# Performance work log

Hardware: AMD Instinct MI355X
Metric: run time of the kernel (lower is better)

Reference implementation:

```python
import jax, jax.numpy as jnp
import numpy as np
import math

B, S, D, H, L, K = 4, 2048, 256, 8, 2, 3  # batch, seq, dim, heads, MTA layers, conv kernel
HS = D // H
EPS = 1e-6


def layer_norm(x, g, b):
    m = jnp.mean(x, axis=-1, keepdims=True)
    v = jnp.mean((x - m) ** 2, axis=-1, keepdims=True)
    return (x - m) * jax.lax.rsqrt(v + EPS) * g + b


def temporal_encoder(x, W, b):
    # x: [B,S,D]; W: [L,K,D,D] (WIO), b: [L,D]. Stack of kernel-3 'SAME' Conv1d, GELU between.
    for i in range(L):
        x = jax.lax.conv_general_dilated(
            x, W[i], window_strides=(1,), padding=[(1, 1)],
            dimension_numbers=("NWC", "WIO", "NWC")) + b[i]
        if i < L - 1:
            x = jax.nn.gelu(x)
    return x


def setup_inputs() -> dict:
    key = jax.random.key(0)
    ks = jax.random.split(key, 10)
    w = lambda k, shape: jax.random.normal(k, shape, jnp.float32) * 0.02
    return {
        "x": jax.random.normal(ks[0], (B, S, D), jnp.float32),
        "ln1_g": jnp.ones((D,), jnp.float32), "ln1_b": jnp.zeros((D,), jnp.float32),
        "Wq": w(ks[1], (L, K, D, D)), "bq": jnp.zeros((L, D), jnp.float32),
        "Wk": w(ks[2], (L, K, D, D)), "bk": jnp.zeros((L, D), jnp.float32),
        "Wv": w(ks[3], (L, K, D, D)), "bv": jnp.zeros((L, D), jnp.float32),
        "ln2_g": jnp.ones((D,), jnp.float32), "ln2_b": jnp.zeros((D,), jnp.float32),
        "Wo1": w(ks[4], (D, D)), "bo1": jnp.zeros((D,), jnp.float32),
        "Wo2": w(ks[5], (D, D)), "bo2": jnp.zeros((D,), jnp.float32),
        "mask": jax.random.randint(ks[6], (B, S), 0, 2).astype(jnp.int32),
    }


def reference(x, ln1_g, ln1_b, Wq, bq, Wk, bk, Wv, bv, ln2_g, ln2_b, Wo1, bo1, Wo2, bo2, mask):
    b_, s_ = x.shape[0], x.shape[1]
    h = layer_norm(x, ln1_g, ln1_b)
    q = temporal_encoder(h, Wq, bq).reshape(b_, s_, H, HS)
    k = temporal_encoder(h, Wk, bk).reshape(b_, s_, H, HS)
    v = temporal_encoder(h, Wv, bv).reshape(b_, s_, H, HS)
    # attention scores [B,H,S,S]
    scores = jnp.einsum("bqhd,bkhd->bhqk", q, k) / math.sqrt(HS)
    m = mask[:, None, None, :].astype(scores.dtype)  # [B,1,1,S]
    scores = scores + (1.0 - m) * (-1e30)
    probs = jax.nn.softmax(scores, axis=-1)
    attn = jnp.einsum("bhqk,bkhd->bqhd", probs, v).reshape(b_, s_, D)
    residual = x + attn  # dropout p=0
    o = layer_norm(residual, ln2_g, ln2_b)
    o = jax.nn.gelu(o @ Wo1 + bo1)  # 1x1 Conv1D == per-token linear
    o = o @ Wo2 + bo2 + residual
    return o
```

## Files before the change

kernel.cpp:

```cpp
#include <hip/hip_runtime.h>
#include <hip/hip_bf16.h>
#include <math.h>

#define BB 4
#define SS 2048
#define DD 256
#define HH 8
#define HSZ 32

typedef __attribute__((ext_vector_type(8))) short short8;
typedef __attribute__((ext_vector_type(4))) float f32x4;

__device__ __forceinline__ void gload_lds16(const void* g, void* l) {
    __builtin_amdgcn_global_load_lds((const unsigned int*)g, (unsigned int*)l,
                                     16, 0, 0);
}

__device__ __forceinline__ float exp2_hw(float x) {
    float r;
    asm("v_exp_f32 %0, %1" : "=v"(r) : "v"(x));
    return r;
}

__device__ __forceinline__ unsigned int perm_pack(float a, float b, unsigned int sel) {
    unsigned int r;
    asm("v_perm_b32 %0, %1, %2, %3"
        : "=v"(r)
        : "v"(__float_as_uint(b)), "v"(__float_as_uint(a)), "s"(sel));
    return r;
}

__device__ __forceinline__ float gelu_f(float x) {
    float x3 = x * x * x;
    float z = 0.7978845608028654f * fmaf(0.044715f, x3, x);
    float e = __expf(2.0f * z);
    float t = 1.0f - 2.0f / (e + 1.0f);
    return 0.5f * x * (1.0f + t);
}

__device__ __forceinline__ unsigned short f2bf(float f) {
    unsigned int u = __float_as_uint(f);
    u = (u + 0x7fffu + ((u >> 16) & 1u)) >> 16;
    return (unsigned short)u;
}

template<bool HASRES>
__device__ __forceinline__ void ln_wave_body(
    int t, int lane,
    const float* __restrict__ x, const float* __restrict__ addin,
    const float* __restrict__ g, const float* __restrict__ bvec,
    float* __restrict__ resid_out, unsigned short* __restrict__ oln_bf)
{
    const int base = t * DD + lane * 4;
    float4 v4 = *(const float4*)&x[base];
    if (HASRES) {
        float4 a4 = *(const float4*)&addin[base];
        v4.x += a4.x; v4.y += a4.y; v4.z += a4.z; v4.w += a4.w;
        *(float4*)&resid_out[base] = v4;
    }
    float s = (v4.x + v4.y) + (v4.z + v4.w);
    #pragma unroll
    for (int o = 1; o < 64; o <<= 1) s += __shfl_xor(s, o);
    float mean = s * (1.0f / 256.0f);
    float dx = v4.x - mean, dy = v4.y - mean, dz = v4.z - mean, dw = v4.w - mean;
    float q = (dx * dx + dy * dy) + (dz * dz + dw * dw);
    #pragma unroll
    for (int o = 1; o < 64; o <<= 1) q += __shfl_xor(q, o);
    float r = rsqrtf(q * (1.0f / 256.0f) + 1e-6f);
    const float4 g4 = *(const float4*)&g[lane * 4];
    const float4 b4 = *(const float4*)&bvec[lane * 4];
    ushort4 o4;
    o4.x = f2bf(dx * r * g4.x + b4.x);
    o4.y = f2bf(dy * r * g4.y + b4.y);
    o4.z = f2bf(dz * r * g4.z + b4.z);
    o4.w = f2bf(dw * r * g4.w + b4.w);
    *(ushort4*)&oln_bf[base] = o4;
}

__global__ __launch_bounds__(256) void prep_kernel(
    const float* __restrict__ Wq, const float* __restrict__ Wk,
    const float* __restrict__ Wv, const float* __restrict__ Wo1,
    const float* __restrict__ Wo2, unsigned short* __restrict__ wt,
    const float* __restrict__ x, const float* __restrict__ ln1g,
    const float* __restrict__ ln1b, unsigned short* __restrict__ h_bf,
    const int* __restrict__ mask, float* __restrict__ maskf)
{
    if (blockIdx.x < 1280) {
        const int WCp = 3 * DD * DD;
        const int WMp = DD * DD;
        const float* src; unsigned short* dst; int rel;
        int i = blockIdx.x;
        if (i < 1152) {
            int seg = i / 192; rel = i % 192;
            src = seg == 0 ? Wq : seg == 1 ? Wq + WCp : seg == 2 ? Wk :
                  seg == 3 ? Wk + WCp : seg == 4 ? Wv : Wv + WCp;
            dst = wt + (size_t)seg * WCp;
        } else {
            int j = i - 1152; int seg = j / 64; rel = j % 64;
            src = seg == 0 ? Wo1 : Wo2;
            dst = wt + (size_t)6 * WCp + (size_t)seg * WMp;
        }
        __shared__ unsigned short t[32][33];
        const int tx = threadIdx.x & 31, ty = threadIdx.x >> 5;
        const int r0 = (rel / 8) * 32, c0 = (rel % 8) * 32;
        #pragma unroll
        for (int j = 0; j < 32; j += 8)
            t[ty + j][tx] = f2bf(src[(r0 + ty + j) * 256 + c0 + tx]);
        __syncthreads();
        #pragma unroll
        for (int j = 0; j < 32; j += 8) {
            unsigned int och = (unsigned int)(c0 + ty + j);
            unsigned int k   = (unsigned int)(r0 + tx);
            unsigned int u   = och * 32u + (k & 31u);
            u ^= ((u >> 6) & 7u) << 3;
            dst[(size_t)(k >> 5) * 8192 + u] = t[tx][ty + j];
        }
    } else if (blockIdx.x < 3328) {
        const int wv = threadIdx.x >> 6, lane = threadIdx.x & 63;
        ln_wave_body<false>((blockIdx.x - 1280) * 4 + wv, lane,
                            x, nullptr, ln1g, ln1b, nullptr, h_bf);
    } else {
        const float M_ON  = -8.0f * 1.4426950408889634f;
        const float M_OFF = -1.442695e30f;
        int i = (blockIdx.x - 3328) * 1024 + threadIdx.x * 4;
        int4 m4 = *(const int4*)&mask[i];
        float4 f4;
        f4.x = m4.x ? M_ON : M_OFF;
        f4.y = m4.y ? M_ON : M_OFF;
        f4.z = m4.z ? M_ON : M_OFF;
        f4.w = m4.w ? M_ON : M_OFF;
        *(float4*)&maskf[i] = f4;
    }
}

__global__ __launch_bounds__(256, 3) void convdual_kernel(
    const unsigned short* __restrict__ in,
    const unsigned short* __restrict__ W0a, const unsigned short* __restrict__ W0b,
    const unsigned short* __restrict__ W0c,
    const unsigned short* __restrict__ W1a, const unsigned short* __restrict__ W1b,
    const unsigned short* __restrict__ W1c,
    const float* __restrict__ ba, const float* __restrict__ bb,
    const float* __restrict__ bc,
    unsigned short* __restrict__ oQ, unsigned short* __restrict__ oK,
    unsigned short* __restrict__ oV, int S)
{
    constexpr int LDW = 264;
    __shared__ __align__(16) unsigned short stage[36 * LDW];
    __shared__ __align__(16) unsigned short wbuf[2][8192];

    unsigned short* const inter = stage;

    const int set = blockIdx.x % 3;
    const int tile = blockIdx.x / 3;
    const unsigned short* W0 = set == 0 ? W0a : (set == 1 ? W0b : W0c);
    const unsigned short* W1 = set == 0 ? W1a : (set == 1 ? W1b : W1c);
    const float* bias         = set == 0 ? ba  : (set == 1 ? bb  : bc);
    unsigned short* outp      = set == 0 ? oQ  : (set == 1 ? oK  : oV);

    const int tid = threadIdx.x;
    const int lane = tid & 63, wv = tid >> 6;
    const int lm = lane & 15, lq = lane >> 4;
    const int tpb = S / 32;
    const int b = tile / tpb;
    const int s0 = (tile % tpb) * 32;
    const int NC = S / 32;
    const int c = s0 >> 5;

    for (int i = tid; i < 36 * 32; i += 256) {
        int r = i >> 5, c8 = (i & 31) << 3;
        int s = s0 + r - 2;
        int4 val = make_int4(0, 0, 0, 0);
        if (s >= 0 && s < S)
            val = *(const int4*)&in[(size_t)(b * S + s) * 256 + c8];
        *(int4*)&stage[r * LDW + c8] = val;
    }

    const int n0 = wv * 64;

    const int wq = wv * 4096;
    const char* w0p = (const char*)W0 + wq + lane * 16;
    const char* w1p = (const char*)W1 + wq + lane * 16;
    char* const wb0 = (char*)wbuf;

    unsigned int boff[4];
    #pragma unroll
    for (int nt = 0; nt < 4; ++nt) {
        unsigned int och = (unsigned int)(n0 + nt * 16 + lm);
        unsigned int R = och * 64u + (unsigned int)lq * 16u;
        boff[nt] = R ^ (((R >> 7) & 7u) << 4);
    }

    __syncthreads();

    {
        f32x4 acc[3][4];
        #pragma unroll
        for (int mt = 0; mt < 3; ++mt)
            #pragma unroll
            for (int nt = 0; nt < 4; ++nt) acc[mt][nt] = (f32x4){0.f, 0.f, 0.f, 0.f};

        #pragma unroll
        for (int j = 0; j < 4; ++j) gload_lds16(w0p + j * 1024,         wb0 + wq + j * 1024);
        #pragma unroll
        for (int j = 0; j < 4; ++j) gload_lds16(w0p + 16384 + j * 1024, wb0 + 16384 + wq + j * 1024);

        short8 a0c, a1c, a2c;
        {
            const int icc0 = lq * 8;
            int r20 = 32 + lm; r20 = r20 > 35 ? 35 : r20;
            a0c = *(const short8*)&stage[lm * LDW + icc0];
            a1c = *(const short8*)&stage[(16 + lm) * LDW + icc0];
            a2c = *(const short8*)&stage[r20 * LDW + icc0];
        }

        asm volatile("s_waitcnt vmcnt(4)" ::: "memory");
        __builtin_amdgcn_sched_barrier(0);
        short8 bfc[4];
        #pragma unroll
        for (int nt = 0; nt < 4; ++nt)
            bfc[nt] = *(const short8*)(wb0 + boff[nt]);

        #pragma unroll
        for (int it = 0; it < 24; ++it) {
            asm volatile("s_waitcnt lgkmcnt(0)" ::: "memory");
            __builtin_amdgcn_sched_barrier(0);
            if (it + 2 < 24) {
                char* ld = wb0 + ((it & 1) << 14) + wq;
                const int soff = (it + 2) * 16384;
                #pragma unroll
                for (int j = 0; j < 4; ++j)
                    gload_lds16(w0p + soff + j * 1024, ld + j * 1024);
            }
            __builtin_amdgcn_sched_barrier(0);

            __builtin_amdgcn_s_setprio(1);
            #pragma unroll
            for (int nt = 0; nt < 4; ++nt) {
                acc[0][nt] = __builtin_amdgcn_mfma_f32_16x16x32_bf16(a0c, bfc[nt], acc[0][nt], 0, 0, 0);
                acc[1][nt] = __builtin_amdgcn_mfma_f32_16x16x32_bf16(a1c, bfc[nt], acc[1][nt], 0, 0, 0);
                acc[2][nt] = __builtin_amdgcn_mfma_f32_16x16x32_bf16(a2c, bfc[nt], acc[2][nt], 0, 0, 0);
            }
            __builtin_amdgcn_s_setprio(0);
            __builtin_amdgcn_sched_barrier(0);

            if (it + 1 < 24) {
                if (it + 2 < 24) { asm volatile("s_waitcnt vmcnt(4)" ::: "memory"); }
                else             { asm volatile("s_waitcnt vmcnt(0)" ::: "memory"); }
                __builtin_amdgcn_sched_barrier(0);
                const char* wb = wb0 + (((it + 1) & 1) << 14);
                #pragma unroll
                for (int nt = 0; nt < 4; ++nt)
                    bfc[nt] = *(const short8*)(wb + boff[nt]);
                const int kk = (it + 1) >> 3;
                const int icc = ((it + 1) & 7) * 32 + lq * 8;
                int r2 = kk + 32 + lm; r2 = r2 > 35 ? 35 : r2;
                a0c = *(const short8*)&stage[(kk + lm) * LDW + icc];
                a1c = *(const short8*)&stage[(kk + 16 + lm) * LDW + icc];
                a2c = *(const short8*)&stage[r2 * LDW + icc];
            }
        }

        __syncthreads();

        #pragma unroll
        for (int j = 0; j < 4; ++j) gload_lds16(w1p + j * 1024,         wb0 + wq + j * 1024);
        #pragma unroll
        for (int j = 0; j < 4; ++j) gload_lds16(w1p + 16384 + j * 1024, wb0 + 16384 + wq + j * 1024);

        #pragma unroll
        for (int mt = 0; mt < 3; ++mt)
            #pragma unroll
            for (int nt = 0; nt < 4; ++nt) {
                int ch = n0 + nt * 16 + lm;
                float bv = bias[ch];
                #pragma unroll
                for (int r = 0; r < 4; ++r) {
                    int j = mt * 16 + lq * 4 + r;
                    if (j < 34) {
                        int token = s0 - 1 + j;
                        unsigned short v = (token >= 0 && token < S)
                            ? f2bf(gelu_f(acc[mt][nt][r] + bv)) : (unsigned short)0;
                        inter[j * LDW + ch] = v;
                    }
                }
            }
    }
    __syncthreads();

    f32x4 acc2[2][4];
    #pragma unroll
    for (int mt = 0; mt < 2; ++mt)
        #pragma unroll
        for (int nt = 0; nt < 4; ++nt) acc2[mt][nt] = (f32x4){0.f, 0.f, 0.f, 0.f};
    {
        char* const wb0 = (char*)wbuf;
        short8 a0c, a1c;
        {
            const int icc0 = lq * 8;
            a0c = *(const short8*)&inter[lm * LDW + icc0];
            a1c = *(const short8*)&inter[(16 + lm) * LDW + icc0];
        }

        asm volatile("s_waitcnt vmcnt(4)" ::: "memory");
        __builtin_amdgcn_sched_barrier(0);
        short8 bfc[4];
        #pragma unroll
        for (int nt = 0; nt < 4; ++nt)
            bfc[nt] = *(const short8*)(wb0 + boff[nt]);

        #pragma unroll
        for (int it = 0; it < 24; ++it) {
            asm volatile("s_waitcnt lgkmcnt(0)" ::: "memory");
            __builtin_amdgcn_sched_barrier(0);
            if (it + 2 < 24) {
                char* ld = wb0 + ((it & 1) << 14) + wq;
                const int soff = (it + 2) * 16384;
                #pragma unroll
                for (int j = 0; j < 4; ++j)
                    gload_lds16(w1p + soff + j * 1024, ld + j * 1024);
            }
            __builtin_amdgcn_sched_barrier(0);

            __builtin_amdgcn_s_setprio(1);
            #pragma unroll
            for (int nt = 0; nt < 4; ++nt) {
                acc2[0][nt] = __builtin_amdgcn_mfma_f32_16x16x32_bf16(a0c, bfc[nt], acc2[0][nt], 0, 0, 0);
                acc2[1][nt] = __builtin_amdgcn_mfma_f32_16x16x32_bf16(a1c, bfc[nt], acc2[1][nt], 0, 0, 0);
            }
            __builtin_amdgcn_s_setprio(0);
            __builtin_amdgcn_sched_barrier(0);

            if (it + 1 < 24) {
                if (it + 2 < 24) { asm volatile("s_waitcnt vmcnt(4)" ::: "memory"); }
                else             { asm volatile("s_waitcnt vmcnt(0)" ::: "memory"); }
                __builtin_amdgcn_sched_barrier(0);
                const char* wb = wb0 + (((it + 1) & 1) << 14);
                #pragma unroll
                for (int nt = 0; nt < 4; ++nt)
                    bfc[nt] = *(const short8*)(wb + boff[nt]);
                const int kk = (it + 1) >> 3;
                const int icc = ((it + 1) & 7) * 32 + lq * 8;
                a0c = *(const short8*)&inter[(kk + lm) * LDW + icc];
                a1c = *(const short8*)&inter[(kk + 16 + lm) * LDW + icc];
            }
        }
    }

    __syncthreads();
    if (set < 2) {
        #pragma unroll
        for (int mt = 0; mt < 2; ++mt)
            #pragma unroll
            for (int nt = 0; nt < 4; ++nt) {
                int o = n0 + nt * 16 + lm;
                int d = o & 31, h = o >> 5;
                float bv = bias[256 + o];
                #pragma unroll
                for (int r = 0; r < 4; ++r) {
                    int t = lq * 4 + r;
                    stage[mt * 4096 + (h * 64 + (d >> 3) * 16 + t) * 8 + (d & 7)] =
                        f2bf(acc2[mt][nt][r] + bv);
                }
            }
        __syncthreads();
        int h = tid >> 5;
        size_t base = ((size_t)(b * 8 + h) * NC + c) * 1024;
        #pragma unroll
        for (int half = 0; half < 2; ++half) {
            int4 v0 = *(const int4*)&stage[half * 4096 + tid * 16];
            int4 v1 = *(const int4*)&stage[half * 4096 + tid * 16 + 8];
            size_t dst = base + half * 512 + (tid & 31) * 16;
            *(int4*)&outp[dst] = v0;
            *(int4*)&outp[dst + 8] = v1;
        }
    } else {
        #pragma unroll
        for (int mt = 0; mt < 2; ++mt)
            #pragma unroll
            for (int nt = 0; nt < 4; ++nt) {
                int o = n0 + nt * 16 + lm;
                int d = o & 31, h = o >> 5;
                float bv = bias[256 + o];
                #pragma unroll
                for (int r = 0; r < 4; ++r) {
                    int t = lq * 4 + r;
                    stage[mt * 4096 +
                          ((h * 2 + (d >> 4)) * 32 + (t >> 3) * 16 + (d & 15)) * 8 + (t & 7)] =
                        f2bf(acc2[mt][nt][r] + bv);
                }
            }
        __syncthreads();
        int h = tid >> 5, dh = (tid >> 4) & 1;
        size_t base = ((size_t)(b * 8 + h) * NC + c) * 1024;
        #pragma unroll
        for (int half = 0; half < 2; ++half) {
            int4 v0 = *(const int4*)&stage[half * 4096 + tid * 16];
            int4 v1 = *(const int4*)&stage[half * 4096 + tid * 16 + 8];
            size_t dst = base + dh * 512 + half * 256 + (tid & 15) * 16;
            *(int4*)&outp[dst] = v0;
            *(int4*)&outp[dst + 8] = v1;
        }
    }
}

__global__ __launch_bounds__(256, 2) void tail_kernel(
    const float* __restrict__ x, const float* __restrict__ attn,
    const float* __restrict__ g2, const float* __restrict__ b2,
    const unsigned short* __restrict__ W1, const float* __restrict__ bo1,
    const unsigned short* __restrict__ W2, const float* __restrict__ bo2,
    float* __restrict__ out, int S)
{
    constexpr int LDW = 264;
    __shared__ __align__(16) unsigned short h_lds[16 * LDW];
    __shared__ __align__(16) unsigned short h2_lds[16 * LDW];
    __shared__ __align__(16) float resid_lds[16][DD];
    __shared__ __align__(16) unsigned short wbuf[2][8192];

    const int tid = threadIdx.x;
    const int lane = tid & 63, wv = tid >> 6;
    const int lm = lane & 15, lq = lane >> 4;
    const int t0 = blockIdx.x * 16;
    const int n0 = wv * 64;

    const int wq = wv * 4096;
    const char* w1p = (const char*)W1 + wq + lane * 16;
    const char* w2p = (const char*)W2 + wq + lane * 16;
    char* const wb0 = (char*)wbuf;

    unsigned int boff[4];
    #pragma unroll
    for (int nt = 0; nt < 4; ++nt) {
        unsigned int och = (unsigned int)(n0 + nt * 16 + lm);
        unsigned int R = och * 64u + (unsigned int)lq * 16u;
        boff[nt] = R ^ (((R >> 7) & 7u) << 4);
    }

    #pragma unroll
    for (int j = 0; j < 4; ++j) gload_lds16(w1p + j * 1024,         wb0 + wq + j * 1024);
    #pragma unroll
    for (int j = 0; j < 4; ++j) gload_lds16(w1p + 16384 + j * 1024, wb0 + 16384 + wq + j * 1024);

    #pragma unroll
    for (int j = 0; j < 4; ++j) {
        int t = wv * 4 + j;
        int base = (t0 + t) * DD + lane * 4;
        float4 v4 = *(const float4*)&x[base];
        float4 a4 = *(const float4*)&attn[base];
        v4.x += a4.x; v4.y += a4.y; v4.z += a4.z; v4.w += a4.w;
        *(float4*)&resid_lds[t][lane * 4] = v4;
        float s = (v4.x + v4.y) + (v4.z + v4.w);
        #pragma unroll
        for (int o = 1; o < 64; o <<= 1) s += __shfl_xor(s, o);
        float mean = s * (1.0f / 256.0f);
        float dx = v4.x - mean, dy = v4.y - mean, dz = v4.z - mean, dw = v4.w - mean;
        float q = (dx * dx + dy * dy) + (dz * dz + dw * dw);
        #pragma unroll
        for (int o = 1; o < 64; o <<= 1) q += __shfl_xor(q, o);
        float r = rsqrtf(q * (1.0f / 256.0f) + 1e-6f);
        const float4 g4 = *(const float4*)&g2[lane * 4];
        const float4 b4 = *(const float4*)&b2[lane * 4];
        ushort4 o4;
        o4.x = f2bf(dx * r * g4.x + b4.x);
        o4.y = f2bf(dy * r * g4.y + b4.y);
        o4.z = f2bf(dz * r * g4.z + b4.z);
        o4.w = f2bf(dw * r * g4.w + b4.w);
        *(ushort4*)&h_lds[t * LDW + lane * 4] = o4;
    }
    __syncthreads();

    {
        f32x4 acc[4];
        #pragma unroll
        for (int nt = 0; nt < 4; ++nt) acc[nt] = (f32x4){0.f, 0.f, 0.f, 0.f};

        short8 a0c = *(const short8*)&h_lds[lm * LDW + lq * 8];
        asm volatile("s_waitcnt vmcnt(4)" ::: "memory");
        __builtin_amdgcn_sched_barrier(0);
        short8 bfc[4];
        #pragma unroll
        for (int nt = 0; nt < 4; ++nt)
            bfc[nt] = *(const short8*)(wb0 + boff[nt]);

        #pragma unroll
        for (int it = 0; it < 8; ++it) {
            asm volatile("s_waitcnt lgkmcnt(0)" ::: "memory");
            __builtin_amdgcn_sched_barrier(0);
            if (it + 2 < 8) {
                char* ld = wb0 + ((it & 1) << 14) + wq;
                const int soff = (it + 2) * 16384;
                #pragma unroll
                for (int j = 0; j < 4; ++j)
                    gload_lds16(w1p + soff + j * 1024, ld + j * 1024);
            }
            __builtin_amdgcn_sched_barrier(0);

            __builtin_amdgcn_s_setprio(1);
            #pragma unroll
            for (int nt = 0; nt < 4; ++nt)
                acc[nt] = __builtin_amdgcn_mfma_f32_16x16x32_bf16(a0c, bfc[nt], acc[nt], 0, 0, 0);
            __builtin_amdgcn_s_setprio(0);
            __builtin_amdgcn_sched_barrier(0);

            if (it + 1 < 8) {
                if (it + 2 < 8) { asm volatile("s_waitcnt vmcnt(4)" ::: "memory"); }
                else            { asm volatile("s_waitcnt vmcnt(0)" ::: "memory"); }
                __builtin_amdgcn_sched_barrier(0);
                const char* wb = wb0 + (((it + 1) & 1) << 14);
                #pragma unroll
                for (int nt = 0; nt < 4; ++nt)
                    bfc[nt] = *(const short8*)(wb + boff[nt]);
                a0c = *(const short8*)&h_lds[lm * LDW + (it + 1) * 32 + lq * 8];
            }
        }

        asm volatile("s_waitcnt lgkmcnt(0)" ::: "memory");
        __builtin_amdgcn_sched_barrier(0);
        #pragma unroll
        for (int j = 0; j < 4; ++j) gload_lds16(w2p + j * 1024,         wb0 + wq + j * 1024);
        #pragma unroll
        for (int j = 0; j < 4; ++j) gload_lds16(w2p + 16384 + j * 1024, wb0 + 16384 + wq + j * 1024);

        #pragma unroll
        for (int nt = 0; nt < 4; ++nt) {
            int ch = n0 + nt * 16 + lm;
            float bv = bo1[ch];
            #pragma unroll
            for (int r = 0; r < 4; ++r) {
                int tok = lq * 4 + r;
                h2_lds[tok * LDW + ch] = f2bf(gelu_f(acc[nt][r] + bv));
            }
        }
    }
    __syncthreads();

    {
        f32x4 acc[4];
        #pragma unroll
        for (int nt = 0; nt < 4; ++nt) acc[nt] = (f32x4){0.f, 0.f, 0.f, 0.f};

        short8 a0c = *(const short8*)&h2_lds[lm * LDW + lq * 8];
        asm volatile("s_waitcnt vmcnt(4)" ::: "memory");
        __builtin_amdgcn_sched_barrier(0);
        short8 bfc[4];
        #pragma unroll
        for (int nt = 0; nt < 4; ++nt)
            bfc[nt] = *(const short8*)(wb0 + boff[nt]);

        #pragma unroll
        for (int it = 0; it < 8; ++it) {
            asm volatile("s_waitcnt lgkmcnt(0)" ::: "memory");
            __builtin_amdgcn_sched_barrier(0);
            if (it + 2 < 8) {
                char* ld = wb0 + ((it & 1) << 14) + wq;
                const int soff = (it + 2) * 16384;
                #pragma unroll
                for (int j = 0; j < 4; ++j)
                    gload_lds16(w2p + soff + j * 1024, ld + j * 1024);
            }
            __builtin_amdgcn_sched_barrier(0);

            __builtin_amdgcn_s_setprio(1);
            #pragma unroll
            for (int nt = 0; nt < 4; ++nt)
                acc[nt] = __builtin_amdgcn_mfma_f32_16x16x32_bf16(a0c, bfc[nt], acc[nt], 0, 0, 0);
            __builtin_amdgcn_s_setprio(0);
            __builtin_amdgcn_sched_barrier(0);

            if (it + 1 < 8) {
                if (it + 2 < 8) { asm volatile("s_waitcnt vmcnt(4)" ::: "memory"); }
                else            { asm volatile("s_waitcnt vmcnt(0)" ::: "memory"); }
                __builtin_amdgcn_sched_barrier(0);
                const char* wb = wb0 + (((it + 1) & 1) << 14);
                #pragma unroll
                for (int nt = 0; nt < 4; ++nt)
                    bfc[nt] = *(const short8*)(wb + boff[nt]);
                a0c = *(const short8*)&h2_lds[lm * LDW + (it + 1) * 32 + lq * 8];
            }
        }
        #pragma unroll
        for (int nt = 0; nt < 4; ++nt) {
            int ch = n0 + nt * 16 + lm;
            float bv = bo2[ch];
            #pragma unroll
            for (int r = 0; r < 4; ++r) {
                int tok = lq * 4 + r;
                out[(size_t)(t0 + tok) * DD + ch] = acc[nt][r] + bv + resid_lds[tok][ch];
            }
        }
    }
}

__global__ __launch_bounds__(256) void attn_mfma_kernel(
    const unsigned short* __restrict__ Qf, const unsigned short* __restrict__ Kf,
    const unsigned short* __restrict__ Vf, const float* __restrict__ maskf,
    float* __restrict__ Out, int S, int H)
{
    constexpr int LDP = 40;
    __shared__ __align__(16) unsigned short p_lds[4][2][16 * LDP];

    const int bh = ((blockIdx.x & 7) << 2) | ((blockIdx.x >> 3) & 3);
    const int qt = (blockIdx.x >> 5) * 128;
    const int b = bh / H;
    const int tid = threadIdx.x;
    const int lane = tid & 63, wv = tid >> 6;
    const int lm = lane & 15, lq = lane >> 4;
    const int q0 = qt + wv * 32;
    const int NC = S / 32;

    const size_t base = (size_t)bh * NC * 1024;
    const unsigned short* qp = &Qf[base + (size_t)(q0 >> 5) * 1024 + lane * 8];
    short8 qf0 = *(const short8*)(qp);
    short8 qf1 = *(const short8*)(qp + 512);
    const unsigned short* kp = Kf + base + lane * 8;
    const unsigned short* vp = Vf + base + lane * 8;

    short8 ones;
    #pragma unroll
    for (int j = 0; j < 8; ++j) ones[j] = (short)0x3F80;

    f32x4 o00 = {0.f, 0.f, 0.f, 0.f}, o01 = {0.f, 0.f, 0.f, 0.f};
    f32x4 o10 = {0.f, 0.f, 0.f, 0.f}, o11 = {0.f, 0.f, 0.f, 0.f};
    f32x4 lacc0 = {0.f, 0.f, 0.f, 0.f}, lacc1 = {0.f, 0.f, 0.f, 0.f};
    const f32x4 zf = {0.f, 0.f, 0.f, 0.f};

    const float scale2 = 0.17677669529663687f * 1.4426950408889634f;
    const unsigned int psel = 0x07060302u;
    const float* mp0 = maskf + b * S + lq * 4;
    const float* mp1 = mp0 + 16;

    unsigned short* pw0 = p_lds[wv][0];
    unsigned short* pw1 = p_lds[wv][1];
    const int pst = lm * LDP + lq * 4;
    const int prd = lm * LDP + lq * 8;

    short8 kA0 = *(const short8*)(kp);
    short8 kA1 = *(const short8*)(kp + 512);
    short8 vA0 = *(const short8*)(vp);
    short8 vA1 = *(const short8*)(vp + 512);
    short8 kB0, kB1, vB0, vB1;

    for (int c = 0; c < NC; c += 2) {
        {
            const unsigned short* kq = kp + (size_t)(c + 1) * 1024;
            const unsigned short* vq = vp + (size_t)(c + 1) * 1024;
            kB0 = *(const short8*)(kq);
            kB1 = *(const short8*)(kq + 512);
            vB0 = *(const short8*)(vq);
            vB1 = *(const short8*)(vq + 512);
        }

        {
            f32x4 s00 = __builtin_amdgcn_mfma_f32_16x16x32_bf16(kA0, qf0, zf, 0, 0, 0);
            f32x4 s01 = __builtin_amdgcn_mfma_f32_16x16x32_bf16(kA1, qf0, zf, 0, 0, 0);
            f32x4 s10 = __builtin_amdgcn_mfma_f32_16x16x32_bf16(kA0, qf1, zf, 0, 0, 0);
            f32x4 s11 = __builtin_amdgcn_mfma_f32_16x16x32_bf16(kA1, qf1, zf, 0, 0, 0);

            float4 mf0 = *(const float4*)(mp0 + c * 32);
            float4 mf1 = *(const float4*)(mp1 + c * 32);

            float p0[8], p1[8];
            p0[0] = exp2_hw(fmaf(s00[0], scale2, mf0.x));
            p0[1] = exp2_hw(fmaf(s00[1], scale2, mf0.y));
            p0[2] = exp2_hw(fmaf(s00[2], scale2, mf0.z));
            p0[3] = exp2_hw(fmaf(s00[3], scale2, mf0.w));
            p0[4] = exp2_hw(fmaf(s01[0], scale2, mf1.x));
            p0[5] = exp2_hw(fmaf(s01[1], scale2, mf1.y));
            p0[6] = exp2_hw(fmaf(s01[2], scale2, mf1.z));
            p0[7] = exp2_hw(fmaf(s01[3], scale2, mf1.w));
            p1[0] = exp2_hw(fmaf(s10[0], scale2, mf0.x));
            p1[1] = exp2_hw(fmaf(s10[1], scale2, mf0.y));
            p1[2] = exp2_hw(fmaf(s10[2], scale2, mf0.z));
            p1[3] = exp2_hw(fmaf(s10[3], scale2, mf0.w));
            p1[4] = exp2_hw(fmaf(s11[0], scale2, mf1.x));
            p1[5] = exp2_hw(fmaf(s11[1], scale2, mf1.y));
            p1[6] = exp2_hw(fmaf(s11[2], scale2, mf1.z));
            p1[7] = exp2_hw(fmaf(s11[3], scale2, mf1.w));

            uint2 w0, w1;
            w0.x = perm_pack(p0[0], p0[1], psel); w0.y = perm_pack(p0[2], p0[3], psel);
            w1.x = perm_pack(p0[4], p0[5], psel); w1.y = perm_pack(p0[6], p0[7], psel);
            *(uint2*)&pw0[pst] = w0;
            *(uint2*)&pw0[pst + 16] = w1;
            w0.x = perm_pack(p1[0], p1[1], psel); w0.y = perm_pack(p1[2], p1[3], psel);
            w1.x = perm_pack(p1[4], p1[5], psel); w1.y = perm_pack(p1[6], p1[7], psel);
            *(uint2*)&pw1[pst] = w0;
            *(uint2*)&pw1[pst + 16] = w1;

            short8 pA0 = *(const short8*)&pw0[prd];
            short8 pA1 = *(const short8*)&pw1[prd];

            lacc0 = __builtin_amdgcn_mfma_f32_16x16x32_bf16(pA0, ones, lacc0, 0, 0, 0);
            o00   = __builtin_amdgcn_mfma_f32_16x16x32_bf16(pA0, vA0, o00, 0, 0, 0);
            o01   = __builtin_amdgcn_mfma_f32_16x16x32_bf16(pA0, vA1, o01, 0, 0, 0);
            lacc1 = __builtin_amdgcn_mfma_f32_16x16x32_bf16(pA1, ones, lacc1, 0, 0, 0);
            o10   = __builtin_amdgcn_mfma_f32_16x16x32_bf16(pA1, vA0, o10, 0, 0, 0);
            o11   = __builtin_amdgcn_mfma_f32_16x16x32_bf16(pA1, vA1, o11, 0, 0, 0);
        }

        if (c + 2 < NC) {
            const unsigned short* kq = kp + (size_t)(c + 2) * 1024;
            const unsigned short* vq = vp + (size_t)(c + 2) * 1024;
            kA0 = *(const short8*)(kq);
            kA1 = *(const short8*)(kq + 512);
            vA0 = *(const short8*)(vq);
            vA1 = *(const short8*)(vq + 512);
        }

        {
            f32x4 s00 = __builtin_amdgcn_mfma_f32_16x16x32_bf16(kB0, qf0, zf, 0, 0, 0);
            f32x4 s01 = __builtin_amdgcn_mfma_f32_16x16x32_bf16(kB1, qf0, zf, 0, 0, 0);
            f32x4 s10 = __builtin_amdgcn_mfma_f32_16x16x32_bf16(kB0, qf1, zf, 0, 0, 0);
            f32x4 s11 = __builtin_amdgcn_mfma_f32_16x16x32_bf16(kB1, qf1, zf, 0, 0, 0);

            float4 mf0 = *(const float4*)(mp0 + (c + 1) * 32);
            float4 mf1 = *(const float4*)(mp1 + (c + 1) * 32);

            float p0[8], p1[8];
            p0[0] = exp2_hw(fmaf(s00[0], scale2, mf0.x));
            p0[1] = exp2_hw(fmaf(s00[1], scale2, mf0.y));
            p0[2] = exp2_hw(fmaf(s00[2], scale2, mf0.z));
            p0[3] = exp2_hw(fmaf(s00[3], scale2, mf0.w));
            p0[4] = exp2_hw(fmaf(s01[0], scale2, mf1.x));
            p0[5] = exp2_hw(fmaf(s01[1], scale2, mf1.y));
            p0[6] = exp2_hw(fmaf(s01[2], scale2, mf1.z));
            p0[7] = exp2_hw(fmaf(s01[3], scale2, mf1.w));
            p1[0] = exp2_hw(fmaf(s10[0], scale2, mf0.x));
            p1[1] = exp2_hw(fmaf(s10[1], scale2, mf0.y));
            p1[2] = exp2_hw(fmaf(s10[2], scale2, mf0.z));
            p1[3] = exp2_hw(fmaf(s10[3], scale2, mf0.w));
            p1[4] = exp2_hw(fmaf(s11[0], scale2, mf1.x));
            p1[5] = exp2_hw(fmaf(s11[1], scale2, mf1.y));
            p1[6] = exp2_hw(fmaf(s11[2], scale2, mf1.z));
            p1[7] = exp2_hw(fmaf(s11[3], scale2, mf1.w));

            uint2 w0, w1;
            w0.x = perm_pack(p0[0], p0[1], psel); w0.y = perm_pack(p0[2], p0[3], psel);
            w1.x = perm_pack(p0[4], p0[5], psel); w1.y = perm_pack(p0[6], p0[7], psel);
            *(uint2*)&pw0[pst] = w0;
            *(uint2*)&pw0[pst + 16] = w1;
            w0.x = perm_pack(p1[0], p1[1], psel); w0.y = perm_pack(p1[2], p1[3], psel);
            w1.x = perm_pack(p1[4], p1[5], psel); w1.y = perm_pack(p1[6], p1[7], psel);
            *(uint2*)&pw1[pst] = w0;
            *(uint2*)&pw1[pst + 16] = w1;

            short8 pA0 = *(const short8*)&pw0[prd];
            short8 pA1 = *(const short8*)&pw1[prd];

            lacc0 = __builtin_amdgcn_mfma_f32_16x16x32_bf16(pA0, ones, lacc0, 0, 0, 0);
            o00   = __builtin_amdgcn_mfma_f32_16x16x32_bf16(pA0, vB0, o00, 0, 0, 0);
            o01   = __builtin_amdgcn_mfma_f32_16x16x32_bf16(pA0, vB1, o01, 0, 0, 0);
            lacc1 = __builtin_amdgcn_mfma_f32_16x16x32_bf16(pA1, ones, lacc1, 0, 0, 0);
            o10   = __builtin_amdgcn_mfma_f32_16x16x32_bf16(pA1, vB0, o10, 0, 0, 0);
            o11   = __builtin_amdgcn_mfma_f32_16x16x32_bf16(pA1, vB1, o11, 0, 0, 0);
        }
    }

    #pragma unroll
    for (int r = 0; r < 4; ++r) {
        float inv0 = 1.0f / lacc0[r];
        size_t ob0 = (size_t)(b * S + q0 + lq * 4 + r) * 256 + (bh % H) * 32;
        Out[ob0 + lm] = o00[r] * inv0;
        Out[ob0 + 16 + lm] = o01[r] * inv0;
        float inv1 = 1.0f / lacc1[r];
        size_t ob1 = (size_t)(b * S + q0 + 16 + lq * 4 + r) * 256 + (bh % H) * 32;
        Out[ob1 + lm] = o10[r] * inv1;
        Out[ob1 + 16 + lm] = o11[r] * inv1;
    }
}

extern "C" void kernel_launch(void* const* d_in, const int* in_sizes, int n_in,
                              void* d_out, int out_size, void* d_ws, size_t ws_size,
                              hipStream_t stream) {
    (void)in_sizes; (void)n_in; (void)out_size; (void)ws_size;
    const float* x    = (const float*)d_in[0];
    const float* ln1g = (const float*)d_in[1];
    const float* ln1b = (const float*)d_in[2];
    const float* Wq   = (const float*)d_in[3];
    const float* bq   = (const float*)d_in[4];
    const float* Wk   = (const float*)d_in[5];
    const float* bk   = (const float*)d_in[6];
    const float* Wv   = (const float*)d_in[7];
    const float* bv   = (const float*)d_in[8];
    const float* ln2g = (const float*)d_in[9];
    const float* ln2b = (const float*)d_in[10];
    const float* Wo1  = (const float*)d_in[11];
    const float* bo1  = (const float*)d_in[12];
    const float* Wo2  = (const float*)d_in[13];
    const float* bo2  = (const float*)d_in[14];
    const int*   mask = (const int*)d_in[15];
    float* out = (float*)d_out;

    const int S = SS, H = HH;
    const int T = BB * SS;
    const size_t NE = (size_t)T * DD;
    float* ws    = (float*)d_ws;
    float* attn  = ws + 0 * NE;
    float* maskf = ws + 1 * NE;
    unsigned short* qf_g  = (unsigned short*)(ws + 2 * NE);
    unsigned short* kf_g  = qf_g + NE;
    unsigned short* h_bf  = kf_g + NE;
    unsigned short* wt    = h_bf + NE;
    const int WC = 3 * DD * DD;
    const int WM = DD * DD;
    unsigned short* wtq0 = wt;
    unsigned short* wtq1 = wt + WC;
    unsigned short* wtk0 = wt + 2 * WC;
    unsigned short* wtk1 = wt + 3 * WC;
    unsigned short* wtv0 = wt + 4 * WC;
    unsigned short* wtv1 = wt + 5 * WC;
    unsigned short* wto1 = wt + 6 * WC;
    unsigned short* wto2 = wt + 6 * WC + WM;
    unsigned short* vf_g = wt + 6 * WC + 2 * WM;

    prep_kernel<<<1280 + T / 4 + 8, 256, 0, stream>>>(
        Wq, Wk, Wv, Wo1, Wo2, wt, x, ln1g, ln1b, h_bf, mask, maskf);

    convdual_kernel<<<(T / 32) * 3, 256, 0, stream>>>(
        h_bf, wtq0, wtk0, wtv0, wtq1, wtk1, wtv1, bq, bk, bv,
        qf_g, kf_g, vf_g, S);

    attn_mfma_kernel<<<BB * H * (S / 128), 256, 0, stream>>>(qf_g, kf_g, vf_g, maskf, attn, S, H);

    tail_kernel<<<T / 16, 256, 0, stream>>>(
        x, attn, ln2g, ln2b, wto1, bo1, wto2, bo2, out, S);
}
```

Measured before the change: 180.6 us.

## Stage shared K/V chunks through double-buffered LDS with direct global-to-LDS loads

Attention K/V tiles were previously loaded by every wave straight from global memory into registers, so the four waves of a block each fetched the same data. Now each wave issues one global_load_lds for a quarter of a 32-key chunk into a double-buffered LDS area, and all waves read K/V from LDS. This cuts redundant global/L2 traffic by four. In exchange it adds two __syncthreads and full vmcnt/lgkmcnt waits per chunk, and prefetch depth drops to one chunk ahead, which may serialize latency.

```diff
diff --git a/kernel.cpp b/kernel.cpp
--- a/kernel.cpp
+++ b/kernel.cpp
@@ -597,6 +597,7 @@
 {
     constexpr int LDP = 40;
     __shared__ __align__(16) unsigned short p_lds[4][2][16 * LDP];
+    __shared__ __align__(16) unsigned short kvbuf[2][2048];
 
     const int bh = ((blockIdx.x & 7) << 2) | ((blockIdx.x >> 3) & 3);
     const int qt = (blockIdx.x >> 5) * 128;
@@ -611,8 +612,11 @@
     const unsigned short* qp = &Qf[base + (size_t)(q0 >> 5) * 1024 + lane * 8];
     short8 qf0 = *(const short8*)(qp);
     short8 qf1 = *(const short8*)(qp + 512);
-    const unsigned short* kp = Kf + base + lane * 8;
-    const unsigned short* vp = Vf + base + lane * 8;
+
+    const char* gsrc = (const char*)(wv < 2 ? Kf + base : Vf + base)
+                       + (wv & 1) * 1024 + (size_t)lane * 16;
+    char* const lb = (char*)kvbuf;
+    const int lseg = wv * 1024;
 
     short8 ones;
     #pragma unroll
@@ -633,126 +637,71 @@
     const int pst = lm * LDP + lq * 4;
     const int prd = lm * LDP + lq * 8;
 
-    short8 kA0 = *(const short8*)(kp);
-    short8 kA1 = *(const short8*)(kp + 512);
-    short8 vA0 = *(const short8*)(vp);
-    short8 vA1 = *(const short8*)(vp + 512);
-    short8 kB0, kB1, vB0, vB1;
-
-    for (int c = 0; c < NC; c += 2) {
-        {
-            const unsigned short* kq = kp + (size_t)(c + 1) * 1024;
-            const unsigned short* vq = vp + (size_t)(c + 1) * 1024;
-            kB0 = *(const short8*)(kq);
-            kB1 = *(const short8*)(kq + 512);
-            vB0 = *(const short8*)(vq);
-            vB1 = *(const short8*)(vq + 512);
-        }
-
-        {
-            f32x4 s00 = __builtin_amdgcn_mfma_f32_16x16x32_bf16(kA0, qf0, zf, 0, 0, 0);
-            f32x4 s01 = __builtin_amdgcn_mfma_f32_16x16x32_bf16(kA1, qf0, zf, 0, 0, 0);
-            f32x4 s10 = __builtin_amdgcn_mfma_f32_16x16x32_bf16(kA0, qf1, zf, 0, 0, 0);
-            f32x4 s11 = __builtin_amdgcn_mfma_f32_16x16x32_bf16(kA1, qf1, zf, 0, 0, 0);
-
-            float4 mf0 = *(const float4*)(mp0 + c * 32);
-            float4 mf1 = *(const float4*)(mp1 + c * 32);
-
-            float p0[8], p1[8];
-            p0[0] = exp2_hw(fmaf(s00[0], scale2, mf0.x));
-            p0[1] = exp2_hw(fmaf(s00[1], scale2, mf0.y));
-            p0[2] = exp2_hw(fmaf(s00[2], scale2, mf0.z));
-            p0[3] = exp2_hw(fmaf(s00[3], scale2, mf0.w));
-            p0[4] = exp2_hw(fmaf(s01[0], scale2, mf1.x));
-            p0[5] = exp2_hw(fmaf(s01[1], scale2, mf1.y));
-            p0[6] = exp2_hw(fmaf(s01[2], scale2, mf1.z));
-            p0[7] = exp2_hw(fmaf(s01[3], scale2, mf1.w));
-            p1[0] = exp2_hw(fmaf(s10[0], scale2, mf0.x));
-            p1[1] = exp2_hw(fmaf(s10[1], scale2, mf0.y));
-            p1[2] = exp2_hw(fmaf(s10[2], scale2, mf0.z));
-            p1[3] = exp2_hw(fmaf(s10[3], scale2, mf0.w));
-            p1[4] = exp2_hw(fmaf(s11[0], scale2, mf1.x));
-            p1[5] = exp2_hw(fmaf(s11[1], scale2, mf1.y));
-            p1[6] = exp2_hw(fmaf(s11[2], scale2, mf1.z));
-            p1[7] = exp2_hw(fmaf(s11[3], scale2, mf1.w));
-
-            uint2 w0, w1;
-            w0.x = perm_pack(p0[0], p0[1], psel); w0.y = perm_pack(p0[2], p0[3], psel);
-            w1.x = perm_pack(p0[4], p0[5], psel); w1.y = perm_pack(p0[6], p0[7], psel);
-            *(uint2*)&pw0[pst] = w0;
-            *(uint2*)&pw0[pst + 16] = w1;
-            w0.x = perm_pack(p1[0], p1[1], psel); w0.y = perm_pack(p1[2], p1[3], psel);
-            w1.x = perm_pack(p1[4], p1[5], psel); w1.y = perm_pack(p1[6], p1[7], psel);
-            *(uint2*)&pw1[pst] = w0;
-            *(uint2*)&pw1[pst + 16] = w1;
-
-            short8 pA0 = *(const short8*)&pw0[prd];
-            short8 pA1 = *(const short8*)&pw1[prd];
-
-            lacc0 = __builtin_amdgcn_mfma_f32_16x16x32_bf16(pA0, ones, lacc0, 0, 0, 0);
-            o00   = __builtin_amdgcn_mfma_f32_16x16x32_bf16(pA0, vA0, o00, 0, 0, 0);
-            o01   = __builtin_amdgcn_mfma_f32_16x16x32_bf16(pA0, vA1, o01, 0, 0, 0);
-            lacc1 = __builtin_amdgcn_mfma_f32_16x16x32_bf16(pA1, ones, lacc1, 0, 0, 0);
-            o10   = __builtin_amdgcn_mfma_f32_16x16x32_bf16(pA1, vA0, o10, 0, 0, 0);
-            o11   = __builtin_amdgcn_mfma_f32_16x16x32_bf16(pA1, vA1, o11, 0, 0, 0);
-        }
-
-        if (c + 2 < NC) {
-            const unsigned short* kq = kp + (size_t)(c + 2) * 1024;
-            const unsigned short* vq = vp + (size_t)(c + 2) * 1024;
-            kA0 = *(const short8*)(kq);
-            kA1 = *(const short8*)(kq + 512);
-            vA0 = *(const short8*)(vq);
-            vA1 = *(const short8*)(vq + 512);
-        }
-
-        {
-            f32x4 s00 = __builtin_amdgcn_mfma_f32_16x16x32_bf16(kB0, qf0, zf, 0, 0, 0);
-            f32x4 s01 = __builtin_amdgcn_mfma_f32_16x16x32_bf16(kB1, qf0, zf, 0, 0, 0);
-            f32x4 s10 = __builtin_amdgcn_mfma_f32_16x16x32_bf16(kB0, qf1, zf, 0, 0, 0);
-            f32x4 s11 = __builtin_amdgcn_mfma_f32_16x16x32_bf16(kB1, qf1, zf, 0, 0, 0);
-
-            float4 mf0 = *(const float4*)(mp0 + (c + 1) * 32);
-            float4 mf1 = *(const float4*)(mp1 + (c + 1) * 32);
-
-            float p0[8], p1[8];
-            p0[0] = exp2_hw(fmaf(s00[0], scale2, mf0.x));
-            p0[1] = exp2_hw(fmaf(s00[1], scale2, mf0.y));
-            p0[2] = exp2_hw(fmaf(s00[2], scale2, mf0.z));
-            p0[3] = exp2_hw(fmaf(s00[3], scale2, mf0.w));
-            p0[4] = exp2_hw(fmaf(s01[0], scale2, mf1.x));
-            p0[5] = exp2_hw(fmaf(s01[1], scale2, mf1.y));
-            p0[6] = exp2_hw(fmaf(s01[2], scale2, mf1.z));
-            p0[7] = exp2_hw(fmaf(s01[3], scale2, mf1.w));
-            p1[0] = exp2_hw(fmaf(s10[0], scale2, mf0.x));
-            p1[1] = exp2_hw(fmaf(s10[1], scale2, mf0.y));
-            p1[2] = exp2_hw(fmaf(s10[2], scale2, mf0.z));
-            p1[3] = exp2_hw(fmaf(s10[3], scale2, mf0.w));
-            p1[4] = exp2_hw(fmaf(s11[0], scale2, mf1.x));
-            p1[5] = exp2_hw(fmaf(s11[1], scale2, mf1.y));
-            p1[6] = exp2_hw(fmaf(s11[2], scale2, mf1.z));
-            p1[7] = exp2_hw(fmaf(s11[3], scale2, mf1.w));
-
-            uint2 w0, w1;
-            w0.x = perm_pack(p0[0], p0[1], psel); w0.y = perm_pack(p0[2], p0[3], psel);
-            w1.x = perm_pack(p0[4], p0[5], psel); w1.y = perm_pack(p0[6], p0[7], psel);
-            *(uint2*)&pw0[pst] = w0;
-            *(uint2*)&pw0[pst + 16] = w1;
-            w0.x = perm_pack(p1[0], p1[1], psel); w0.y = perm_pack(p1[2], p1[3], psel);
-            w1.x = perm_pack(p1[4], p1[5], psel); w1.y = perm_pack(p1[6], p1[7], psel);
-            *(uint2*)&pw1[pst] = w0;
-            *(uint2*)&pw1[pst + 16] = w1;
-
-            short8 pA0 = *(const short8*)&pw0[prd];
-            short8 pA1 = *(const short8*)&pw1[prd];
-
-            lacc0 = __builtin_amdgcn_mfma_f32_16x16x32_bf16(pA0, ones, lacc0, 0, 0, 0);
-            o00   = __builtin_amdgcn_mfma_f32_16x16x32_bf16(pA0, vB0, o00, 0, 0, 0);
-            o01   = __builtin_amdgcn_mfma_f32_16x16x32_bf16(pA0, vB1, o01, 0, 0, 0);
-            lacc1 = __builtin_amdgcn_mfma_f32_16x16x32_bf16(pA1, ones, lacc1, 0, 0, 0);
-            o10   = __builtin_amdgcn_mfma_f32_16x16x32_bf16(pA1, vB0, o10, 0, 0, 0);
-            o11   = __builtin_amdgcn_mfma_f32_16x16x32_bf16(pA1, vB1, o11, 0, 0, 0);
-        }
+    gload_lds16(gsrc,        lb + lseg);
+    gload_lds16(gsrc + 2048, lb + 4096 + lseg);
+
+    for (int c = 0; c < NC; ++c) {
+        asm volatile("s_waitcnt vmcnt(0)" ::: "memory");
+        __builtin_amdgcn_sched_barrier(0);
+        __syncthreads();
+
+        const char* kb = lb + ((c & 1) << 12);
+        short8 k0 = *(const short8*)(kb + (size_t)lane * 16);
+        short8 k1 = *(const short8*)(kb + 1024 + (size_t)lane * 16);
+        short8 v0 = *(const short8*)(kb + 2048 + (size_t)lane * 16);
+        short8 v1 = *(const short8*)(kb + 3072 + (size_t)lane * 16);
+        asm volatile("s_waitcnt lgkmcnt(0)" ::: "memory");
+        __builtin_amdgcn_sched_barrier(0);
+        __syncthreads();
+
+        if (c + 2 < NC)
+            gload_lds16(gsrc + (size_t)(c + 2) * 2048, lb + ((c & 1) << 12) + lseg);
+
+        f32x4 s00 = __builtin_amdgcn_mfma_f32_16x16x32_bf16(k0, qf0, zf, 0, 0, 0);
+        f32x4 s01 = __builtin_amdgcn_mfma_f32_16x16x32_bf16(k1, qf0, zf, 0, 0, 0);
+        f32x4 s10 = __builtin_amdgcn_mfma_f32_16x16x32_bf16(k0, qf1, zf, 0, 0, 0);
+        f32x4 s11 = __builtin_amdgcn_mfma_f32_16x16x32_bf16(k1, qf1, zf, 0, 0, 0);
+
+        float4 mf0 = *(const float4*)(mp0 + c * 32);
+        float4 mf1 = *(const float4*)(mp1 + c * 32);
+
+        float p0[8], p1[8];
+        p0[0] = exp2_hw(fmaf(s00[0], scale2, mf0.x));
+        p0[1] = exp2_hw(fmaf(s00[1], scale2, mf0.y));
+        p0[2] = exp2_hw(fmaf(s00[2], scale2, mf0.z));
+        p0[3] = exp2_hw(fmaf(s00[3], scale2, mf0.w));
+        p0[4] = exp2_hw(fmaf(s01[0], scale2, mf1.x));
+        p0[5] = exp2_hw(fmaf(s01[1], scale2, mf1.y));
+        p0[6] = exp2_hw(fmaf(s01[2], scale2, mf1.z));
+        p0[7] = exp2_hw(fmaf(s01[3], scale2, mf1.w));
+        p1[0] = exp2_hw(fmaf(s10[0], scale2, mf0.x));
+        p1[1] = exp2_hw(fmaf(s10[1], scale2, mf0.y));
+        p1[2] = exp2_hw(fmaf(s10[2], scale2, mf0.z));
+        p1[3] = exp2_hw(fmaf(s10[3], scale2, mf0.w));
+        p1[4] = exp2_hw(fmaf(s11[0], scale2, mf1.x));
+        p1[5] = exp2_hw(fmaf(s11[1], scale2, mf1.y));
+        p1[6] = exp2_hw(fmaf(s11[2], scale2, mf1.z));
+        p1[7] = exp2_hw(fmaf(s11[3], scale2, mf1.w));
+
+        uint2 w0, w1;
+        w0.x = perm_pack(p0[0], p0[1], psel); w0.y = perm_pack(p0[2], p0[3], psel);
+        w1.x = perm_pack(p0[4], p0[5], psel); w1.y = perm_pack(p0[6], p0[7], psel);
+        *(uint2*)&pw0[pst] = w0;
+        *(uint2*)&pw0[pst + 16] = w1;
+        w0.x = perm_pack(p1[0], p1[1], psel); w0.y = perm_pack(p1[2], p1[3], psel);
+        w1.x = perm_pack(p1[4], p1[5], psel); w1.y = perm_pack(p1[6], p1[7], psel);
+        *(uint2*)&pw1[pst] = w0;
+        *(uint2*)&pw1[pst + 16] = w1;
+
+        short8 pA0 = *(const short8*)&pw0[prd];
+        short8 pA1 = *(const short8*)&pw1[prd];
+
+        lacc0 = __builtin_amdgcn_mfma_f32_16x16x32_bf16(pA0, ones, lacc0, 0, 0, 0);
+        o00   = __builtin_amdgcn_mfma_f32_16x16x32_bf16(pA0, v0, o00, 0, 0, 0);
+        o01   = __builtin_amdgcn_mfma_f32_16x16x32_bf16(pA0, v1, o01, 0, 0, 0);
+        lacc1 = __builtin_amdgcn_mfma_f32_16x16x32_bf16(pA1, ones, lacc1, 0, 0, 0);
+        o10   = __builtin_amdgcn_mfma_f32_16x16x32_bf16(pA1, v0, o10, 0, 0, 0);
+        o11   = __builtin_amdgcn_mfma_f32_16x16x32_bf16(pA1, v1, o11, 0, 0, 0);
     }
 
     #pragma unroll
```

Result: slower. 188.8 us (+4.5%).
